# Performance work log

Measured on AMD Instinct MI355X. Metric: run time of the kernel, lower is better.

## Reference

```python
import jax, jax.numpy as jnp
import numpy as np

ALPHA = 0.4
STEPS = 4
EPSILON = 0.005

N_NODES = 4096
N_EDGES = 131072
D_FEAT = 128


def setup_inputs() -> dict:
    key = jax.random.key(0)
    k1, k2, k3, k4 = jax.random.split(key, 4)
    x = jax.random.normal(k1, (N_NODES, D_FEAT), dtype=jnp.float32)
    src = jax.random.randint(k2, (N_EDGES,), 0, N_NODES)
    dst = jax.random.randint(k3, (N_EDGES,), 0, N_NODES)
    edge_index = jnp.stack([src, dst], axis=0).astype(jnp.int64)
    edge_attr = jax.random.uniform(k4, (N_EDGES,), dtype=jnp.float32)
    return {"x": x, "edge_index": edge_index, "edge_attr": edge_attr}


def reference(x, edge_index, edge_attr):
    # PPR power series: result = sum_i theta_i * A_i, where
    #   A_0 = edge pattern with unit values, A_1 = A (edge_attr),
    #   A_{i+1} = threshold_eps(A @ A_i).
    # Dense [N,N] representation: thresholding (dropping entries < eps in the
    # sparse original) is exactly zeroing those entries here; jit-compatible
    # since sparse nnz is data-dependent.
    N = x.shape[0]
    src, dst = edge_index[0], edge_index[1]
    A = jnp.zeros((N, N), dtype=edge_attr.dtype).at[src, dst].add(edge_attr)
    P0 = jnp.zeros((N, N), dtype=edge_attr.dtype).at[src, dst].add(1.0)

    mats = [P0, A]
    for _ in range(1, STEPS - 1):
        M = A @ mats[-1]
        M = jnp.where(M >= EPSILON, M, jnp.zeros((), dtype=M.dtype))
        mats.append(M)

    thetas = [ALPHA * (1.0 - ALPHA) ** i for i in range(STEPS)]
    out = thetas[0] * mats[0]
    for t, m in zip(thetas[1:], mats[1:]):
        out = out + t * m
    return out
```

## Files before the change

### kernel.cpp

```cpp
#include <hip/hip_runtime.h>

#define N_NODES 4096
#define EPS 0.005f
#define TH0 0.4f
#define TH1 0.24f
#define TH2 0.144f
#define TH3 0.0864f
#define JTILE 512
#define NTILES (N_NODES / JTILE)
#define RCAP 80

typedef float v4f __attribute__((ext_vector_type(4)));
typedef unsigned short u16x8 __attribute__((ext_vector_type(8)));


static __device__ __forceinline__ float bf2f(unsigned short u) {
    union { unsigned int i; float f; } x;
    x.i = ((unsigned int)u) << 16;
    return x.f;
}

static __device__ __forceinline__ unsigned short f2bf(float f) {
    union { float f; unsigned int i; } x;
    x.f = f;
    unsigned int r = x.i + 0x7fff + ((x.i >> 16) & 1u);
    return (unsigned short)(r >> 16);
}

__global__ void scatter_kernel(const int* __restrict__ idx,
                               const float* __restrict__ attr, int E,
                               int* __restrict__ counts, int* __restrict__ col,
                               float* __restrict__ val) {
    int e = blockIdx.x * blockDim.x + threadIdx.x;
    if (e < E) {
        int s = idx[e];
        int d = idx[e + E];
        int pos = atomicAdd(&counts[s], 1);
        if (pos < RCAP) {
            col[s * RCAP + pos] = d;
            val[s * RCAP + pos] = attr[e];
        }
    }
}

__global__ __launch_bounds__(256)
void m2_kernel(const int* __restrict__ counts, const int* __restrict__ col,
               const float* __restrict__ val, unsigned short* __restrict__ m2) {
    __shared__ float acc[N_NODES];
    __shared__ int   kcol[RCAP];
    __shared__ float kval[RCAP];
    __shared__ int   kcnt[RCAP];
    int i = blockIdx.x;
    int t = threadIdx.x;
    float4 z = make_float4(0.f, 0.f, 0.f, 0.f);
    for (int j4 = t; j4 < N_NODES / 4; j4 += 256) ((float4*)acc)[j4] = z;
    int cnt = min(counts[i], RCAP);
    if (t < cnt) {
        int k = col[i * RCAP + t];
        kcol[t] = k;
        kval[t] = val[i * RCAP + t];
        kcnt[t] = min(counts[k], RCAP);
    }
    __syncthreads();
    int gid = t >> 3, gl = t & 7;
    for (int q = gid; q < cnt; q += 32) {
        float a = kval[q];
        int fb = kcol[q] * RCAP;
        int fn = kcnt[q];
        for (int f = gl; f < fn; f += 8) {
            unsafeAtomicAdd(&acc[col[fb + f]], a * val[fb + f]);
        }
    }
    __syncthreads();
    size_t rb = (size_t)i * N_NODES;
    for (int j4 = t; j4 < N_NODES / 4; j4 += 256) {
        float4 v = ((const float4*)acc)[j4];
        ushort4 r;
        r.x = (v.x >= EPS) ? f2bf(v.x) : (unsigned short)0;
        r.y = (v.y >= EPS) ? f2bf(v.y) : (unsigned short)0;
        r.z = (v.z >= EPS) ? f2bf(v.z) : (unsigned short)0;
        r.w = (v.w >= EPS) ? f2bf(v.w) : (unsigned short)0;
        ((ushort4*)(m2 + rb))[j4] = r;
    }
}

__global__ __launch_bounds__(128)
void out_kernel(const int* __restrict__ counts, const int* __restrict__ col,
                const float* __restrict__ val,
                const unsigned short* __restrict__ m2,
                float* __restrict__ out) {
    int lin = blockIdx.x;
    int tile = lin & 7;
    int jb = tile * JTILE;
    int t = threadIdx.x;
    int w = t >> 6, lane = t & 63;
    int i = 2 * (lin >> 3) + w;
    int cnt = min(counts[i], RCAP);
    int cnt4 = (cnt + 3) & ~3;
    const int*   ci = col + i * RCAP;
    const float* vi = val + i * RCAP;
    const unsigned short* m2l = m2 + jb + 8 * lane;
    v4f acc0 = 0.f, acc1 = 0.f;
    for (int e = 0; e < cnt4; e += 4) {
        int4   kq = *(const int4*)(ci + e);
        float4 aq = *(const float4*)(vi + e);
        int k0 = __builtin_amdgcn_readfirstlane(kq.x);
        int k1 = __builtin_amdgcn_readfirstlane(kq.y);
        int k2 = __builtin_amdgcn_readfirstlane(kq.z);
        int k3 = __builtin_amdgcn_readfirstlane(kq.w);
        u16x8 u0 = *(const u16x8*)(m2l + (size_t)k0 * N_NODES);
        u16x8 u1 = *(const u16x8*)(m2l + (size_t)k1 * N_NODES);
        u16x8 u2 = *(const u16x8*)(m2l + (size_t)k2 * N_NODES);
        u16x8 u3 = *(const u16x8*)(m2l + (size_t)k3 * N_NODES);
        acc0.x = fmaf(aq.x, bf2f(u0[0]), acc0.x);
        acc0.y = fmaf(aq.x, bf2f(u0[1]), acc0.y);
        acc0.z = fmaf(aq.x, bf2f(u0[2]), acc0.z);
        acc0.w = fmaf(aq.x, bf2f(u0[3]), acc0.w);
        acc1.x = fmaf(aq.x, bf2f(u0[4]), acc1.x);
        acc1.y = fmaf(aq.x, bf2f(u0[5]), acc1.y);
        acc1.z = fmaf(aq.x, bf2f(u0[6]), acc1.z);
        acc1.w = fmaf(aq.x, bf2f(u0[7]), acc1.w);
        acc0.x = fmaf(aq.y, bf2f(u1[0]), acc0.x);
        acc0.y = fmaf(aq.y, bf2f(u1[1]), acc0.y);
        acc0.z = fmaf(aq.y, bf2f(u1[2]), acc0.z);
        acc0.w = fmaf(aq.y, bf2f(u1[3]), acc0.w);
        acc1.x = fmaf(aq.y, bf2f(u1[4]), acc1.x);
        acc1.y = fmaf(aq.y, bf2f(u1[5]), acc1.y);
        acc1.z = fmaf(aq.y, bf2f(u1[6]), acc1.z);
        acc1.w = fmaf(aq.y, bf2f(u1[7]), acc1.w);
        acc0.x = fmaf(aq.z, bf2f(u2[0]), acc0.x);
        acc0.y = fmaf(aq.z, bf2f(u2[1]), acc0.y);
        acc0.z = fmaf(aq.z, bf2f(u2[2]), acc0.z);
        acc0.w = fmaf(aq.z, bf2f(u2[3]), acc0.w);
        acc1.x = fmaf(aq.z, bf2f(u2[4]), acc1.x);
        acc1.y = fmaf(aq.z, bf2f(u2[5]), acc1.y);
        acc1.z = fmaf(aq.z, bf2f(u2[6]), acc1.z);
        acc1.w = fmaf(aq.z, bf2f(u2[7]), acc1.w);
        acc0.x = fmaf(aq.w, bf2f(u3[0]), acc0.x);
        acc0.y = fmaf(aq.w, bf2f(u3[1]), acc0.y);
        acc0.z = fmaf(aq.w, bf2f(u3[2]), acc0.z);
        acc0.w = fmaf(aq.w, bf2f(u3[3]), acc0.w);
        acc1.x = fmaf(aq.w, bf2f(u3[4]), acc1.x);
        acc1.y = fmaf(aq.w, bf2f(u3[5]), acc1.y);
        acc1.z = fmaf(aq.w, bf2f(u3[6]), acc1.z);
        acc1.w = fmaf(aq.w, bf2f(u3[7]), acc1.w);
    }
    u16x8 um = *(const u16x8*)(m2 + (size_t)i * N_NODES + jb + 8 * lane);
    v4f r0, r1;
    r0.x = TH2 * bf2f(um[0]) + TH3 * ((acc0.x >= EPS) ? acc0.x : 0.0f);
    r0.y = TH2 * bf2f(um[1]) + TH3 * ((acc0.y >= EPS) ? acc0.y : 0.0f);
    r0.z = TH2 * bf2f(um[2]) + TH3 * ((acc0.z >= EPS) ? acc0.z : 0.0f);
    r0.w = TH2 * bf2f(um[3]) + TH3 * ((acc0.w >= EPS) ? acc0.w : 0.0f);
    r1.x = TH2 * bf2f(um[4]) + TH3 * ((acc1.x >= EPS) ? acc1.x : 0.0f);
    r1.y = TH2 * bf2f(um[5]) + TH3 * ((acc1.y >= EPS) ? acc1.y : 0.0f);
    r1.z = TH2 * bf2f(um[6]) + TH3 * ((acc1.z >= EPS) ? acc1.z : 0.0f);
    r1.w = TH2 * bf2f(um[7]) + TH3 * ((acc1.w >= EPS) ? acc1.w : 0.0f);
    float* o = out + (size_t)i * N_NODES + jb + 8 * lane;
    __builtin_nontemporal_store(r0, (v4f*)o);
    __builtin_nontemporal_store(r1, (v4f*)(o + 4));
}

__global__ void edge_epilogue(const int* __restrict__ idx,
                              const float* __restrict__ attr, int E,
                              float* __restrict__ out) {
    int e = blockIdx.x * blockDim.x + threadIdx.x;
    if (e < E) {
        int s = idx[e];
        int d = idx[e + E];
        unsafeAtomicAdd(&out[(size_t)s * N_NODES + d], TH0 + TH1 * attr[e]);
    }
}

extern "C" void kernel_launch(void* const* d_in, const int* in_sizes, int n_in,
                              void* d_out, int out_size, void* d_ws, size_t ws_size,
                              hipStream_t stream) {
    const int* idx = (const int*)d_in[1];
    const float* attr = (const float*)d_in[2];
    int E = in_sizes[1] / 2;

    char* ws = (char*)d_ws;
    int*   counts = (int*)(ws);
    int*   col    = (int*)(ws + (64 << 10));
    float* val    = (float*)(ws + (64 << 10) + N_NODES * RCAP * sizeof(int));
    unsigned short* m2 = (unsigned short*)(ws + (4 << 20));
    float* out    = (float*)d_out;

    (void)hipMemsetAsync(counts, 0, N_NODES * sizeof(int), stream);
    (void)hipMemsetAsync(col, 0, 2 * N_NODES * RCAP * sizeof(int), stream);
    scatter_kernel<<<(E + 255) / 256, 256, 0, stream>>>(idx, attr, E, counts, col, val);
    m2_kernel<<<N_NODES, 256, 0, stream>>>(counts, col, val, m2);
    out_kernel<<<(N_NODES / 2) * NTILES, 128, 0, stream>>>(counts, col, val, m2, out);
    edge_epilogue<<<(E + 255) / 256, 256, 0, stream>>>(idx, attr, E, out);
}
```

Measured before the change: 194.0 us.

## Interleave CSR col/val into pairs and fuse edge epilogue into output kernel

Stores each edge's column and weight as one int2 pair so m2 and out kernels fetch both with a single load. The separate edge_epilogue atomic kernel is removed: each out_kernel block builds its row's P0/A contribution in a shared-memory tile with LDS atomics and adds it before the streaming store. The main accumulation loop is unrolled to 8 neighbours per iteration for more memory-level parallelism, and the two memsets are merged into one. This removes a kernel launch and global atomics on the output, at the cost of extra shared memory and a per-block scan of the row's edges.

```diff
diff --git a/kernel.cpp b/kernel.cpp
--- a/kernel.cpp
+++ b/kernel.cpp
@@ -29,23 +29,25 @@
 
 __global__ void scatter_kernel(const int* __restrict__ idx,
                                const float* __restrict__ attr, int E,
-                               int* __restrict__ counts, int* __restrict__ col,
-                               float* __restrict__ val) {
+                               int* __restrict__ counts, int2* __restrict__ pairs) {
     int e = blockIdx.x * blockDim.x + threadIdx.x;
     if (e < E) {
         int s = idx[e];
         int d = idx[e + E];
+        float a = attr[e];
         int pos = atomicAdd(&counts[s], 1);
         if (pos < RCAP) {
-            col[s * RCAP + pos] = d;
-            val[s * RCAP + pos] = attr[e];
+            int2 p;
+            p.x = d;
+            p.y = __float_as_int(a);
+            pairs[s * RCAP + pos] = p;
         }
     }
 }
 
 __global__ __launch_bounds__(256)
-void m2_kernel(const int* __restrict__ counts, const int* __restrict__ col,
-               const float* __restrict__ val, unsigned short* __restrict__ m2) {
+void m2_kernel(const int* __restrict__ counts, const int2* __restrict__ pairs,
+               unsigned short* __restrict__ m2) {
     __shared__ float acc[N_NODES];
     __shared__ int   kcol[RCAP];
     __shared__ float kval[RCAP];
@@ -56,10 +58,10 @@
     for (int j4 = t; j4 < N_NODES / 4; j4 += 256) ((float4*)acc)[j4] = z;
     int cnt = min(counts[i], RCAP);
     if (t < cnt) {
-        int k = col[i * RCAP + t];
-        kcol[t] = k;
-        kval[t] = val[i * RCAP + t];
-        kcnt[t] = min(counts[k], RCAP);
+        int2 p = pairs[i * RCAP + t];
+        kcol[t] = p.x;
+        kval[t] = __int_as_float(p.y);
+        kcnt[t] = min(counts[p.x], RCAP);
     }
     __syncthreads();
     int gid = t >> 3, gl = t & 7;
@@ -68,7 +70,8 @@
         int fb = kcol[q] * RCAP;
         int fn = kcnt[q];
         for (int f = gl; f < fn; f += 8) {
-            unsafeAtomicAdd(&acc[col[fb + f]], a * val[fb + f]);
+            int2 p = pairs[fb + f];
+            unsafeAtomicAdd(&acc[p.x], a * __int_as_float(p.y));
         }
     }
     __syncthreads();
@@ -85,90 +88,83 @@
 }
 
 __global__ __launch_bounds__(128)
-void out_kernel(const int* __restrict__ counts, const int* __restrict__ col,
-                const float* __restrict__ val,
+void out_kernel(const int* __restrict__ counts, const int2* __restrict__ pairs,
                 const unsigned short* __restrict__ m2,
                 float* __restrict__ out) {
+    __shared__ float ap[2][JTILE];
     int lin = blockIdx.x;
     int tile = lin & 7;
     int jb = tile * JTILE;
     int t = threadIdx.x;
     int w = t >> 6, lane = t & 63;
     int i = 2 * (lin >> 3) + w;
+    float* apw = ap[w];
+    ((float4*)apw)[lane] = make_float4(0.f, 0.f, 0.f, 0.f);
+    ((float4*)apw)[64 + lane] = make_float4(0.f, 0.f, 0.f, 0.f);
     int cnt = min(counts[i], RCAP);
-    int cnt4 = (cnt + 3) & ~3;
-    const int*   ci = col + i * RCAP;
-    const float* vi = val + i * RCAP;
+    const int2* pi = pairs + i * RCAP;
+    for (int e = lane; e < cnt; e += 64) {
+        int2 p = pi[e];
+        int cl = p.x - jb;
+        if ((unsigned)cl < (unsigned)JTILE)
+            unsafeAtomicAdd(&apw[cl], TH0 + TH1 * __int_as_float(p.y));
+    }
+    int cnt8 = (cnt + 7) & ~7;
     const unsigned short* m2l = m2 + jb + 8 * lane;
     v4f acc0 = 0.f, acc1 = 0.f;
-    for (int e = 0; e < cnt4; e += 4) {
-        int4   kq = *(const int4*)(ci + e);
-        float4 aq = *(const float4*)(vi + e);
-        int k0 = __builtin_amdgcn_readfirstlane(kq.x);
-        int k1 = __builtin_amdgcn_readfirstlane(kq.y);
-        int k2 = __builtin_amdgcn_readfirstlane(kq.z);
-        int k3 = __builtin_amdgcn_readfirstlane(kq.w);
+    for (int e = 0; e < cnt8; e += 8) {
+        int4 q01 = *(const int4*)(pi + e);
+        int4 q23 = *(const int4*)(pi + e + 2);
+        int4 q45 = *(const int4*)(pi + e + 4);
+        int4 q67 = *(const int4*)(pi + e + 6);
+        int k0 = __builtin_amdgcn_readfirstlane(q01.x);
+        int k1 = __builtin_amdgcn_readfirstlane(q01.z);
+        int k2 = __builtin_amdgcn_readfirstlane(q23.x);
+        int k3 = __builtin_amdgcn_readfirstlane(q23.z);
+        int k4 = __builtin_amdgcn_readfirstlane(q45.x);
+        int k5 = __builtin_amdgcn_readfirstlane(q45.z);
+        int k6 = __builtin_amdgcn_readfirstlane(q67.x);
+        int k7 = __builtin_amdgcn_readfirstlane(q67.z);
+        float a0 = __int_as_float(q01.y), a1 = __int_as_float(q01.w);
+        float a2 = __int_as_float(q23.y), a3 = __int_as_float(q23.w);
+        float a4 = __int_as_float(q45.y), a5 = __int_as_float(q45.w);
+        float a6 = __int_as_float(q67.y), a7 = __int_as_float(q67.w);
         u16x8 u0 = *(const u16x8*)(m2l + (size_t)k0 * N_NODES);
         u16x8 u1 = *(const u16x8*)(m2l + (size_t)k1 * N_NODES);
         u16x8 u2 = *(const u16x8*)(m2l + (size_t)k2 * N_NODES);
         u16x8 u3 = *(const u16x8*)(m2l + (size_t)k3 * N_NODES);
-        acc0.x = fmaf(aq.x, bf2f(u0[0]), acc0.x);
-        acc0.y = fmaf(aq.x, bf2f(u0[1]), acc0.y);
-        acc0.z = fmaf(aq.x, bf2f(u0[2]), acc0.z);
-        acc0.w = fmaf(aq.x, bf2f(u0[3]), acc0.w);
-        acc1.x = fmaf(aq.x, bf2f(u0[4]), acc1.x);
-        acc1.y = fmaf(aq.x, bf2f(u0[5]), acc1.y);
-        acc1.z = fmaf(aq.x, bf2f(u0[6]), acc1.z);
-        acc1.w = fmaf(aq.x, bf2f(u0[7]), acc1.w);
-        acc0.x = fmaf(aq.y, bf2f(u1[0]), acc0.x);
-        acc0.y = fmaf(aq.y, bf2f(u1[1]), acc0.y);
-        acc0.z = fmaf(aq.y, bf2f(u1[2]), acc0.z);
-        acc0.w = fmaf(aq.y, bf2f(u1[3]), acc0.w);
-        acc1.x = fmaf(aq.y, bf2f(u1[4]), acc1.x);
-        acc1.y = fmaf(aq.y, bf2f(u1[5]), acc1.y);
-        acc1.z = fmaf(aq.y, bf2f(u1[6]), acc1.z);
-        acc1.w = fmaf(aq.y, bf2f(u1[7]), acc1.w);
-        acc0.x = fmaf(aq.z, bf2f(u2[0]), acc0.x);
-        acc0.y = fmaf(aq.z, bf2f(u2[1]), acc0.y);
-        acc0.z = fmaf(aq.z, bf2f(u2[2]), acc0.z);
-        acc0.w = fmaf(aq.z, bf2f(u2[3]), acc0.w);
-        acc1.x = fmaf(aq.z, bf2f(u2[4]), acc1.x);
-        acc1.y = fmaf(aq.z, bf2f(u2[5]), acc1.y);
-        acc1.z = fmaf(aq.z, bf2f(u2[6]), acc1.z);
-        acc1.w = fmaf(aq.z, bf2f(u2[7]), acc1.w);
-        acc0.x = fmaf(aq.w, bf2f(u3[0]), acc0.x);
-        acc0.y = fmaf(aq.w, bf2f(u3[1]), acc0.y);
-        acc0.z = fmaf(aq.w, bf2f(u3[2]), acc0.z);
-        acc0.w = fmaf(aq.w, bf2f(u3[3]), acc0.w);
-        acc1.x = fmaf(aq.w, bf2f(u3[4]), acc1.x);
-        acc1.y = fmaf(aq.w, bf2f(u3[5]), acc1.y);
-        acc1.z = fmaf(aq.w, bf2f(u3[6]), acc1.z);
-        acc1.w = fmaf(aq.w, bf2f(u3[7]), acc1.w);
+        u16x8 u4 = *(const u16x8*)(m2l + (size_t)k4 * N_NODES);
+        u16x8 u5 = *(const u16x8*)(m2l + (size_t)k5 * N_NODES);
+        u16x8 u6 = *(const u16x8*)(m2l + (size_t)k6 * N_NODES);
+        u16x8 u7 = *(const u16x8*)(m2l + (size_t)k7 * N_NODES);
+#define ACC8(uu, aa)                                   \
+        acc0.x = fmaf(aa, bf2f(uu[0]), acc0.x);        \
+        acc0.y = fmaf(aa, bf2f(uu[1]), acc0.y);        \
+        acc0.z = fmaf(aa, bf2f(uu[2]), acc0.z);        \
+        acc0.w = fmaf(aa, bf2f(uu[3]), acc0.w);        \
+        acc1.x = fmaf(aa, bf2f(uu[4]), acc1.x);        \
+        acc1.y = fmaf(aa, bf2f(uu[5]), acc1.y);        \
+        acc1.z = fmaf(aa, bf2f(uu[6]), acc1.z);        \
+        acc1.w = fmaf(aa, bf2f(uu[7]), acc1.w);
+        ACC8(u0, a0) ACC8(u1, a1) ACC8(u2, a2) ACC8(u3, a3)
+        ACC8(u4, a4) ACC8(u5, a5) ACC8(u6, a6) ACC8(u7, a7)
+#undef ACC8
     }
     u16x8 um = *(const u16x8*)(m2 + (size_t)i * N_NODES + jb + 8 * lane);
+    float4 p0 = ((const float4*)apw)[2 * lane];
+    float4 p1 = ((const float4*)apw)[2 * lane + 1];
     v4f r0, r1;
-    r0.x = TH2 * bf2f(um[0]) + TH3 * ((acc0.x >= EPS) ? acc0.x : 0.0f);
-    r0.y = TH2 * bf2f(um[1]) + TH3 * ((acc0.y >= EPS) ? acc0.y : 0.0f);
-    r0.z = TH2 * bf2f(um[2]) + TH3 * ((acc0.z >= EPS) ? acc0.z : 0.0f);
-    r0.w = TH2 * bf2f(um[3]) + TH3 * ((acc0.w >= EPS) ? acc0.w : 0.0f);
-    r1.x = TH2 * bf2f(um[4]) + TH3 * ((acc1.x >= EPS) ? acc1.x : 0.0f);
-    r1.y = TH2 * bf2f(um[5]) + TH3 * ((acc1.y >= EPS) ? acc1.y : 0.0f);
-    r1.z = TH2 * bf2f(um[6]) + TH3 * ((acc1.z >= EPS) ? acc1.z : 0.0f);
-    r1.w = TH2 * bf2f(um[7]) + TH3 * ((acc1.w >= EPS) ? acc1.w : 0.0f);
+    r0.x = p0.x + TH2 * bf2f(um[0]) + TH3 * ((acc0.x >= EPS) ? acc0.x : 0.0f);
+    r0.y = p0.y + TH2 * bf2f(um[1]) + TH3 * ((acc0.y >= EPS) ? acc0.y : 0.0f);
+    r0.z = p0.z + TH2 * bf2f(um[2]) + TH3 * ((acc0.z >= EPS) ? acc0.z : 0.0f);
+    r0.w = p0.w + TH2 * bf2f(um[3]) + TH3 * ((acc0.w >= EPS) ? acc0.w : 0.0f);
+    r1.x = p1.x + TH2 * bf2f(um[4]) + TH3 * ((acc1.x >= EPS) ? acc1.x : 0.0f);
+    r1.y = p1.y + TH2 * bf2f(um[5]) + TH3 * ((acc1.y >= EPS) ? acc1.y : 0.0f);
+    r1.z = p1.z + TH2 * bf2f(um[6]) + TH3 * ((acc1.z >= EPS) ? acc1.z : 0.0f);
+    r1.w = p1.w + TH2 * bf2f(um[7]) + TH3 * ((acc1.w >= EPS) ? acc1.w : 0.0f);
     float* o = out + (size_t)i * N_NODES + jb + 8 * lane;
     __builtin_nontemporal_store(r0, (v4f*)o);
     __builtin_nontemporal_store(r1, (v4f*)(o + 4));
-}
-
-__global__ void edge_epilogue(const int* __restrict__ idx,
-                              const float* __restrict__ attr, int E,
-                              float* __restrict__ out) {
-    int e = blockIdx.x * blockDim.x + threadIdx.x;
-    if (e < E) {
-        int s = idx[e];
-        int d = idx[e + E];
-        unsafeAtomicAdd(&out[(size_t)s * N_NODES + d], TH0 + TH1 * attr[e]);
-    }
 }
 
 extern "C" void kernel_launch(void* const* d_in, const int* in_sizes, int n_in,
@@ -179,16 +175,13 @@
     int E = in_sizes[1] / 2;
 
     char* ws = (char*)d_ws;
-    int*   counts = (int*)(ws);
-    int*   col    = (int*)(ws + (64 << 10));
-    float* val    = (float*)(ws + (64 << 10) + N_NODES * RCAP * sizeof(int));
+    int*  counts = (int*)(ws);
+    int2* pairs  = (int2*)(ws + (16 << 10));
     unsigned short* m2 = (unsigned short*)(ws + (4 << 20));
-    float* out    = (float*)d_out;
+    float* out   = (float*)d_out;
 
-    (void)hipMemsetAsync(counts, 0, N_NODES * sizeof(int), stream);
-    (void)hipMemsetAsync(col, 0, 2 * N_NODES * RCAP * sizeof(int), stream);
-    scatter_kernel<<<(E + 255) / 256, 256, 0, stream>>>(idx, attr, E, counts, col, val);
-    m2_kernel<<<N_NODES, 256, 0, stream>>>(counts, col, val, m2);
-    out_kernel<<<(N_NODES / 2) * NTILES, 128, 0, stream>>>(counts, col, val, m2, out);
-    edge_epilogue<<<(E + 255) / 256, 256, 0, stream>>>(idx, attr, E, out);
+    (void)hipMemsetAsync(ws, 0, (16 << 10) + N_NODES * RCAP * sizeof(int2), stream);
+    scatter_kernel<<<(E + 255) / 256, 256, 0, stream>>>(idx, attr, E, counts, pairs);
+    m2_kernel<<<N_NODES, 256, 0, stream>>>(counts, pairs, m2);
+    out_kernel<<<(N_NODES / 2) * NTILES, 128, 0, stream>>>(counts, pairs, m2, out);
 }
```

Result: faster. 182.5 us (-5.9%).
